# Kernel optimization log

Hardware: AMD Instinct MI355X
Metric: run time of the kernel (lower is better)

## Reference

```python
import jax, jax.numpy as jnp
import numpy as np

N = 262144      # total nodes in disjoint batch
E = 4194304     # total edges (COO)
G = 4096        # number of graphs
DIN = 1
CH = 32


def setup_inputs() -> dict:
    key = jax.random.key(0)
    ks = jax.random.split(key, 16)
    inp = {
        "x": jax.random.uniform(ks[0], (N, DIN), dtype=jnp.float32),
        "edge_src": jax.random.randint(ks[1], (E,), 0, N, dtype=jnp.int32),
        "edge_dst": jax.random.randint(ks[2], (E,), 0, N, dtype=jnp.int32),
        "edge_w": jax.random.uniform(ks[3], (E,), dtype=jnp.float32),  # normalized-adj values
        "seg": jnp.sort(jax.random.randint(ks[4], (N,), 0, G, dtype=jnp.int32)),
        "W1_1": jax.random.normal(ks[5], (DIN, CH), dtype=jnp.float32) * 0.5,
        "W2_1": jax.random.normal(ks[6], (DIN, CH), dtype=jnp.float32) * 0.5,
        "b1": jnp.zeros((CH,), jnp.float32),
        "W1_2": jax.random.normal(ks[7], (CH, CH), dtype=jnp.float32) * (1.0 / np.sqrt(CH)),
        "W2_2": jax.random.normal(ks[8], (CH, CH), dtype=jnp.float32) * (1.0 / np.sqrt(CH)),
        "b2": jnp.zeros((CH,), jnp.float32),
        "W1_3": jax.random.normal(ks[9], (CH, CH), dtype=jnp.float32) * (1.0 / np.sqrt(CH)),
        "W2_3": jax.random.normal(ks[10], (CH, CH), dtype=jnp.float32) * (1.0 / np.sqrt(CH)),
        "b3": jnp.zeros((CH,), jnp.float32),
        "Wd": jax.random.normal(ks[11], (CH, 1), dtype=jnp.float32) * (1.0 / np.sqrt(CH)),
        "bd": jnp.zeros((1,), jnp.float32),
    }
    return inp


def gcs_conv(x, src, dst, w, W1, W2, b):
    # GCSConv: out = relu(A_hat @ (x W1) + x W2 + b), A_hat sparse COO
    h = x @ W1                                   # [N, CH]
    msg = h[src] * w[:, None]                    # gather + edge weight [E, CH]
    agg = jax.ops.segment_sum(msg, dst, num_segments=N)  # scatter-add [N, CH]
    return jax.nn.relu(agg + x @ W2 + b)


def reference(x, edge_src, edge_dst, edge_w, seg,
              W1_1, W2_1, b1, W1_2, W2_2, b2, W1_3, W2_3, b3, Wd, bd):
    x = gcs_conv(x, edge_src, edge_dst, edge_w, W1_1, W2_1, b1)
    x = gcs_conv(x, edge_src, edge_dst, edge_w, W1_2, W2_2, b2)
    x = gcs_conv(x, edge_src, edge_dst, edge_w, W1_3, W2_3, b3)
    # GlobalAvgPool over graph segments
    sums = jax.ops.segment_sum(x, seg, num_segments=G)           # [G, CH]
    counts = jax.ops.segment_sum(jnp.ones((x.shape[0],), x.dtype), seg, num_segments=G)
    pooled = sums / jnp.maximum(counts, 1.0)[:, None]            # [G, CH]
    return jax.nn.sigmoid(pooled @ Wd + bd)                      # [G, 1]
```

## Files before the change

### kernel.cpp

```cpp
#include <hip/hip_runtime.h>
#include <hip/hip_bf16.h>
#include <hip/hip_fp8.h>

#define CH 32
#define BSHIFT 10
#define BNODES (1 << BSHIFT)
#define MAXBUK 256
#define P3_CHUNK 2048
#define CAPB_REC 17408
#define NT 32
#define CAP 768

__device__ __forceinline__ float fp8_to_f32(unsigned int b) {
    __hip_fp8_e4m3 v; v.__x = (__hip_fp8_storage_t)b; return (float)v;
}
__device__ __forceinline__ unsigned char f32_to_fp8(float f) {
    return (unsigned char)__hip_fp8_e4m3(f).__x;
}
__device__ __forceinline__ int2 nt_load_int2(const int2* p) {
    long long raw = __builtin_nontemporal_load(reinterpret_cast<const long long*>(p));
    return make_int2((int)(unsigned int)raw, (int)(raw >> 32));
}


__global__ void init_tails_kernel(int* __restrict__ bucketTail, int nbuk) {
    int tid = threadIdx.x;
    if (tid < nbuk) bucketTail[tid] = tid * CAPB_REC;
}

__global__ void bucket_scatter_kernel(const int* __restrict__ src, const int* __restrict__ dst,
                                      const float* __restrict__ w, int* __restrict__ bucketTail,
                                      int2* __restrict__ rec, int E, int nbuk) {
    __shared__ int cnt[MAXBUK], base[MAXBUK], offs[MAXBUK];
    int tid = threadIdx.x;
    int begin = blockIdx.x * P3_CHUNK;
    int end = min(begin + P3_CHUNK, E);
    if (tid < MAXBUK) cnt[tid] = 0;
    __syncthreads();
    for (int e = begin + tid; e < end; e += 256)
        atomicAdd(&cnt[dst[e] >> BSHIFT], 1);
    __syncthreads();
    if (tid < nbuk) {
        base[tid] = cnt[tid] ? atomicAdd(&bucketTail[tid], cnt[tid]) : 0;
        offs[tid] = 0;
    }
    __syncthreads();
    for (int e = begin + tid; e < end; e += 256) {
        int d = dst[e];
        int b = d >> BSHIFT;
        int p = base[b] + atomicAdd(&offs[b], 1);
        rec[p] = make_int2(src[e] | ((d & (BNODES - 1)) << 18), __float_as_int(w[e]));
    }
}

__global__ void bucket_scan2_kernel(const int* __restrict__ bucketTail, int* __restrict__ bucketStart,
                                    int* __restrict__ row_start, int nbuk, int N, int E) {
    __shared__ int l[MAXBUK];
    int tid = threadIdx.x;
    int v = (tid < nbuk) ? (bucketTail[tid] - tid * CAPB_REC) : 0;
    l[tid] = v;
    __syncthreads();
    for (int off = 1; off < MAXBUK; off <<= 1) {
        int t = (tid >= off) ? l[tid - off] : 0;
        __syncthreads();
        l[tid] += t;
        __syncthreads();
    }
    int ex = l[tid] - v;
    if (tid < nbuk) bucketStart[tid] = ex;
    if (tid == nbuk - 1) bucketStart[nbuk] = ex + v;
    if (tid == 0) row_start[N] = E;
}

__global__ void local_csr_kernel(const int2* __restrict__ rec, const int* __restrict__ bucketStart,
                                 const int* __restrict__ bucketTail,
                                 int* __restrict__ row_start, int2* __restrict__ colw, int N) {
    int b = blockIdx.x;
    int lo_rec = b * CAPB_REC, hi_rec = bucketTail[b];
    int dstBase = bucketStart[b];
    int nodeBase = b << BSHIFT;
    int nNodes = min(BNODES, N - nodeBase);
    __shared__ int deg[BNODES];
    __shared__ int rs[BNODES];
    __shared__ int l[256];
    int tid = threadIdx.x;
    for (int i = tid; i < BNODES; i += 256) deg[i] = 0;
    __syncthreads();
    for (int j = lo_rec + tid; j < hi_rec; j += 256)
        atomicAdd(&deg[rec[j].x >> 18], 1);
    __syncthreads();
    int i0 = tid * 4;
    int v0 = deg[i0], v1 = deg[i0 + 1], v2 = deg[i0 + 2], v3 = deg[i0 + 3];
    int tsum = v0 + v1 + v2 + v3;
    l[tid] = tsum;
    __syncthreads();
    for (int off = 1; off < 256; off <<= 1) {
        int t = (tid >= off) ? l[tid - off] : 0;
        __syncthreads();
        l[tid] += t;
        __syncthreads();
    }
    int ex = l[tid] - tsum;
    rs[i0] = ex; rs[i0 + 1] = ex + v0; rs[i0 + 2] = ex + v0 + v1; rs[i0 + 3] = ex + v0 + v1 + v2;
    __syncthreads();
    for (int i = tid; i < nNodes; i += 256) row_start[nodeBase + i] = dstBase + rs[i];
    for (int i = tid; i < BNODES; i += 256) deg[i] = 0;
    __syncthreads();
    for (int j = lo_rec + tid; j < hi_rec; j += 256) {
        int2 r = rec[j];
        int dl = r.x >> 18;
        int p = dstBase + rs[dl] + atomicAdd(&deg[dl], 1);
        colw[p] = make_int2(r.x & 0x3FFFF, r.y);
    }
}

__global__ void l1_fused_kernel(const float* __restrict__ x,
                                const int* __restrict__ row_start, const int2* __restrict__ colw,
                                const float* __restrict__ W11, const float* __restrict__ W21,
                                const float* __restrict__ b1, const float* __restrict__ W12,
                                float* __restrict__ x1, unsigned char* __restrict__ h2, int N) {
    __shared__ float w1s[CH][CH];
    __shared__ float xs[8][CH + 1];
    int tid = threadIdx.x;
    for (int t = tid; t < CH * CH; t += 256) w1s[t >> 5][t & 31] = W12[t];
    int ln = tid >> 5, c = tid & 31;
    int node = blockIdx.x * 8 + ln;
    float s = 0.f, xv = 0.f;
    if (node < N) {
        xv = x[node];
        int lo = row_start[node], hi = row_start[node + 1];
        for (int j = lo + c; j < hi; j += 32) {
            int2 cw = nt_load_int2(&colw[j]);
            s += __int_as_float(cw.y) * x[cw.x];
        }
    }
    for (int m = 1; m < 32; m <<= 1) s += __shfl_xor(s, m);
    float x1v = 0.f;
    if (node < N) {
        x1v = fmaxf(fmaf(s, W11[c], fmaf(xv, W21[c], b1[c])), 0.f);
        x1[(size_t)node * CH + c] = x1v;
    }
    xs[ln][c] = x1v;
    __syncthreads();
    if (node < N) {
        float a = 0.f;
#pragma unroll
        for (int k = 0; k < CH; k++) a = fmaf(xs[ln][k], w1s[k][c], a);
        h2[(size_t)node * CH + c] = f32_to_fp8(a);
    }
}

template <bool EMIT_H>
__global__ void gather_kernel(float* __restrict__ xio, const unsigned char* __restrict__ h,
                              const int* __restrict__ row_start, const int2* __restrict__ colw,
                              const float* __restrict__ W2, const float* __restrict__ b,
                              const float* __restrict__ W1next, unsigned char* __restrict__ hout,
                              int N) {
    __shared__ float w2s[CH][CH];
    __shared__ float w1s[EMIT_H ? CH : 1][CH];
    __shared__ float xs[NT][CH + 1];
    __shared__ int2 cws[CAP];
    int tid = threadIdx.x;
    int nodeBase = blockIdx.x * NT;

    for (int t = tid; t < CH * CH; t += 256) {
        w2s[t >> 5][t & 31] = W2[t];
        if (EMIT_H) w1s[t >> 5][t & 31] = W1next[t];
    }
    {
        int n = tid >> 5, c = tid & 31;
        for (int p = 0; p < NT / 8; p++) {
            int node = nodeBase + p * 8 + n;
            xs[p * 8 + n][c] = (node < N) ? __builtin_nontemporal_load(&xio[(size_t)node * CH + c]) : 0.f;
        }
    }
    int lo = row_start[min(nodeBase, N)];
    int hi = row_start[min(nodeBase + NT, N)];
    int total = hi - lo;
    int cnt = min(total, CAP);
    for (int t = tid; t < cnt; t += 256) cws[t] = nt_load_int2(&colw[lo + t]);
    __syncthreads();

    int grp = tid >> 4, l16 = tid & 15;
    int c0 = l16 * 2;
#pragma unroll
    for (int rep = 0; rep < NT / 16; rep++) {
        int nloc = rep * 16 + grp;
        int node = nodeBase + nloc;
        if (node < N) {
            int ls = row_start[node], le = row_start[node + 1];
            float a0 = b[c0], a1 = b[c0 + 1];
#pragma unroll
            for (int k = 0; k < CH; k++) {
                float xk = xs[nloc][k];
                float2 wk = *reinterpret_cast<const float2*>(&w2s[k][c0]);
                a0 = fmaf(xk, wk.x, a0);
                a1 = fmaf(xk, wk.y, a1);
            }
            if (total <= cnt) {
                int j = ls;
                for (; j + 4 <= le; j += 4) {
                    int2 e0 = cws[j - lo], e1 = cws[j + 1 - lo], e2 = cws[j + 2 - lo], e3 = cws[j + 3 - lo];
                    unsigned int p0 = *reinterpret_cast<const unsigned short*>(h + (size_t)e0.x * CH + c0);
                    unsigned int p1 = *reinterpret_cast<const unsigned short*>(h + (size_t)e1.x * CH + c0);
                    unsigned int p2 = *reinterpret_cast<const unsigned short*>(h + (size_t)e2.x * CH + c0);
                    unsigned int p3 = *reinterpret_cast<const unsigned short*>(h + (size_t)e3.x * CH + c0);
                    float w0 = __int_as_float(e0.y), w1 = __int_as_float(e1.y);
                    float w2 = __int_as_float(e2.y), w3 = __int_as_float(e3.y);
                    a0 = fmaf(w0, fp8_to_f32(p0 & 0xff), a0); a1 = fmaf(w0, fp8_to_f32(p0 >> 8), a1);
                    a0 = fmaf(w1, fp8_to_f32(p1 & 0xff), a0); a1 = fmaf(w1, fp8_to_f32(p1 >> 8), a1);
                    a0 = fmaf(w2, fp8_to_f32(p2 & 0xff), a0); a1 = fmaf(w2, fp8_to_f32(p2 >> 8), a1);
                    a0 = fmaf(w3, fp8_to_f32(p3 & 0xff), a0); a1 = fmaf(w3, fp8_to_f32(p3 >> 8), a1);
                }
                for (; j < le; j++) {
                    int2 e = cws[j - lo];
                    unsigned int p = *reinterpret_cast<const unsigned short*>(h + (size_t)e.x * CH + c0);
                    float wj = __int_as_float(e.y);
                    a0 = fmaf(wj, fp8_to_f32(p & 0xff), a0); a1 = fmaf(wj, fp8_to_f32(p >> 8), a1);
                }
            } else {
                for (int j = ls; j < le; j++) {
                    int2 e = nt_load_int2(&colw[j]);
                    unsigned int p = *reinterpret_cast<const unsigned short*>(h + (size_t)e.x * CH + c0);
                    float wj = __int_as_float(e.y);
                    a0 = fmaf(wj, fp8_to_f32(p & 0xff), a0); a1 = fmaf(wj, fp8_to_f32(p >> 8), a1);
                }
            }
            float r0 = fmaxf(a0, 0.f), r1 = fmaxf(a1, 0.f);
            size_t oidx = (size_t)node * CH + c0;
            __builtin_nontemporal_store(r0, &xio[oidx]);
            __builtin_nontemporal_store(r1, &xio[oidx + 1]);
            if (EMIT_H) { xs[nloc][c0] = r0; xs[nloc][c0 + 1] = r1; }
        }
    }
    if (EMIT_H) {
        __syncthreads();
#pragma unroll
        for (int rep = 0; rep < NT / 16; rep++) {
            int nloc = rep * 16 + grp;
            int node = nodeBase + nloc;
            if (node >= N) continue;
            float a0 = 0.f, a1 = 0.f;
#pragma unroll
            for (int k = 0; k < CH; k++) {
                float xk = xs[nloc][k];
                float2 wk = *reinterpret_cast<const float2*>(&w1s[k][c0]);
                a0 = fmaf(xk, wk.x, a0);
                a1 = fmaf(xk, wk.y, a1);
            }
            unsigned short pk = (unsigned short)f32_to_fp8(a0) |
                                ((unsigned short)f32_to_fp8(a1) << 8);
            __builtin_nontemporal_store(pk,
                reinterpret_cast<unsigned short*>(hout + (size_t)node * CH + c0));
        }
    }
}

__global__ void pool_head_kernel(const float* __restrict__ x3, const int* __restrict__ seg,
                                 const float* __restrict__ Wd, const float* __restrict__ bd,
                                 float* __restrict__ out, int N, int G) {
    int g = blockIdx.x;
    int tid = threadIdx.x;
    int lo = 0, hi = N;
    while (lo < hi) { int mid = (lo + hi) >> 1; if (seg[mid] < g) lo = mid + 1; else hi = mid; }
    int start = lo;
    hi = N;
    while (lo < hi) { int mid = (lo + hi) >> 1; if (seg[mid] < g + 1) lo = mid + 1; else hi = mid; }
    int end = lo;
    int half = tid >> 5, c = tid & 31;
    float s = 0.f;
    for (int nn = start + half; nn < end; nn += 2)
        s += __builtin_nontemporal_load(&x3[(size_t)nn * CH + c]);
    s += __shfl_xor(s, 32);
    float t = s * Wd[c];
    for (int m = 1; m < 32; m <<= 1) t += __shfl_xor(t, m);
    if (tid == 0) {
        float cntf = fmaxf((float)(end - start), 1.f);
        float logit = t / cntf + bd[0];
        out[g] = 1.f / (1.f + expf(-logit));
    }
}

extern "C" void kernel_launch(void* const* d_in, const int* in_sizes, int n_in,
                              void* d_out, int out_size, void* d_ws, size_t ws_size,
                              hipStream_t stream) {
    const float* x        = (const float*)d_in[0];
    const int*   edge_src = (const int*)d_in[1];
    const int*   edge_dst = (const int*)d_in[2];
    const float* edge_w   = (const float*)d_in[3];
    const int*   seg      = (const int*)d_in[4];
    const float* W1_1 = (const float*)d_in[5];
    const float* W2_1 = (const float*)d_in[6];
    const float* b1   = (const float*)d_in[7];
    const float* W1_2 = (const float*)d_in[8];
    const float* W2_2 = (const float*)d_in[9];
    const float* b2   = (const float*)d_in[10];
    const float* W1_3 = (const float*)d_in[11];
    const float* W2_3 = (const float*)d_in[12];
    const float* b3   = (const float*)d_in[13];
    const float* Wd   = (const float*)d_in[14];
    const float* bd   = (const float*)d_in[15];
    float* out = (float*)d_out;

    const int N = in_sizes[0];
    const int E = in_sizes[1];
    const int G = out_size;
    (void)ws_size; (void)n_in;

    const int nbuk = (N + BNODES - 1) >> BSHIFT;

    const size_t NB = (size_t)N * CH;
    float*           xbuf      = (float*)d_ws;
    int2*            rec       = (int2*)d_ws;
    unsigned char*   h8a       = (unsigned char*)(xbuf + NB);
    unsigned char*   h8b       = h8a + NB;
    int*             row_start = (int*)(h8b + NB);
    int2*            colw      = (int2*)(row_start + (N + 8));
    int*             bucketStart = (int*)(colw + E);
    int*             bucketTail  = bucketStart + MAXBUK + 4;

    const int BLK = 256;

    init_tails_kernel<<<1, BLK, 0, stream>>>(bucketTail, nbuk);
    bucket_scatter_kernel<<<(E + P3_CHUNK - 1) / P3_CHUNK, BLK, 0, stream>>>(
        edge_src, edge_dst, edge_w, bucketTail, rec, E, nbuk);
    bucket_scan2_kernel<<<1, BLK, 0, stream>>>(bucketTail, bucketStart, row_start, nbuk, N, E);
    local_csr_kernel<<<nbuk, BLK, 0, stream>>>(rec, bucketStart, bucketTail, row_start, colw, N);

    l1_fused_kernel<<<(N + 7) / 8, BLK, 0, stream>>>(x, row_start, colw,
                                                     W1_1, W2_1, b1, W1_2, xbuf, h8a, N);
    gather_kernel<true><<<(N + NT - 1) / NT, BLK, 0, stream>>>(xbuf, h8a, row_start, colw,
                                                               W2_2, b2, W1_3, h8b, N);
    gather_kernel<false><<<(N + NT - 1) / NT, BLK, 0, stream>>>(xbuf, h8b, row_start, colw,
                                                                W2_3, b3, nullptr, nullptr, N);

    pool_head_kernel<<<G, 64, 0, stream>>>(xbuf, seg, Wd, bd, out, N, G);
}
```

Before: 473.9 us.

## Split gather into two source-half passes to improve cache locality of fp8 features

```diff
diff --git a/kernel.cpp b/kernel.cpp
--- a/kernel.cpp
+++ b/kernel.cpp
@@ -6,7 +6,7 @@
 #define BSHIFT 10
 #define BNODES (1 << BSHIFT)
 #define MAXBUK 256
-#define P3_CHUNK 2048
+#define P3_CHUNK 8192
 #define CAPB_REC 17408
 #define NT 32
 #define CAP 768
@@ -74,24 +74,28 @@
 
 __global__ void local_csr_kernel(const int2* __restrict__ rec, const int* __restrict__ bucketStart,
                                  const int* __restrict__ bucketTail,
-                                 int* __restrict__ row_start, int2* __restrict__ colw, int N) {
+                                 int* __restrict__ row_start, int* __restrict__ row_mid,
+                                 int2* __restrict__ colw, int N, int halfN) {
     int b = blockIdx.x;
     int lo_rec = b * CAPB_REC, hi_rec = bucketTail[b];
     int dstBase = bucketStart[b];
     int nodeBase = b << BSHIFT;
     int nNodes = min(BNODES, N - nodeBase);
-    __shared__ int deg[BNODES];
-    __shared__ int rs[BNODES];
+    __shared__ int degA[BNODES], degB[BNODES], rs[BNODES], bofs[BNODES];
     __shared__ int l[256];
     int tid = threadIdx.x;
-    for (int i = tid; i < BNODES; i += 256) deg[i] = 0;
-    __syncthreads();
-    for (int j = lo_rec + tid; j < hi_rec; j += 256)
-        atomicAdd(&deg[rec[j].x >> 18], 1);
+    for (int i = tid; i < BNODES; i += 256) { degA[i] = 0; degB[i] = 0; }
+    __syncthreads();
+    for (int j = lo_rec + tid; j < hi_rec; j += 256) {
+        int rx = rec[j].x;
+        int dl = rx >> 18;
+        atomicAdd(((rx & 0x3FFFF) < halfN) ? &degA[dl] : &degB[dl], 1);
+    }
     __syncthreads();
     int i0 = tid * 4;
-    int v0 = deg[i0], v1 = deg[i0 + 1], v2 = deg[i0 + 2], v3 = deg[i0 + 3];
-    int tsum = v0 + v1 + v2 + v3;
+    int t0 = degA[i0] + degB[i0], t1 = degA[i0 + 1] + degB[i0 + 1];
+    int t2 = degA[i0 + 2] + degB[i0 + 2], t3 = degA[i0 + 3] + degB[i0 + 3];
+    int tsum = t0 + t1 + t2 + t3;
     l[tid] = tsum;
     __syncthreads();
     for (int off = 1; off < 256; off <<= 1) {
@@ -101,16 +105,23 @@
         __syncthreads();
     }
     int ex = l[tid] - tsum;
-    rs[i0] = ex; rs[i0 + 1] = ex + v0; rs[i0 + 2] = ex + v0 + v1; rs[i0 + 3] = ex + v0 + v1 + v2;
-    __syncthreads();
-    for (int i = tid; i < nNodes; i += 256) row_start[nodeBase + i] = dstBase + rs[i];
-    for (int i = tid; i < BNODES; i += 256) deg[i] = 0;
+    rs[i0] = ex; rs[i0 + 1] = ex + t0; rs[i0 + 2] = ex + t0 + t1; rs[i0 + 3] = ex + t0 + t1 + t2;
+    __syncthreads();
+    for (int i = tid; i < BNODES; i += 256) bofs[i] = rs[i] + degA[i];
+    __syncthreads();
+    for (int i = tid; i < nNodes; i += 256) {
+        row_start[nodeBase + i] = dstBase + rs[i];
+        row_mid[nodeBase + i]   = dstBase + bofs[i];
+    }
+    for (int i = tid; i < BNODES; i += 256) { degA[i] = 0; degB[i] = 0; }
     __syncthreads();
     for (int j = lo_rec + tid; j < hi_rec; j += 256) {
         int2 r = rec[j];
         int dl = r.x >> 18;
-        int p = dstBase + rs[dl] + atomicAdd(&deg[dl], 1);
-        colw[p] = make_int2(r.x & 0x3FFFF, r.y);
+        int s = r.x & 0x3FFFF;
+        int p = (s < halfN) ? dstBase + rs[dl] + atomicAdd(&degA[dl], 1)
+                            : dstBase + bofs[dl] + atomicAdd(&degB[dl], 1);
+        colw[p] = make_int2(s, r.y);
     }
 }
 
@@ -150,24 +161,25 @@
     }
 }
 
-template <bool EMIT_H>
+template <int PHASE, bool EMIT_H>
 __global__ void gather_kernel(float* __restrict__ xio, const unsigned char* __restrict__ h,
-                              const int* __restrict__ row_start, const int2* __restrict__ colw,
+                              const int* __restrict__ row_start, const int* __restrict__ row_mid,
+                              const int2* __restrict__ colw,
                               const float* __restrict__ W2, const float* __restrict__ b,
                               const float* __restrict__ W1next, unsigned char* __restrict__ hout,
                               int N) {
-    __shared__ float w2s[CH][CH];
+    __shared__ float w2s[PHASE == 0 ? CH : 1][CH];
     __shared__ float w1s[EMIT_H ? CH : 1][CH];
     __shared__ float xs[NT][CH + 1];
     __shared__ int2 cws[CAP];
     int tid = threadIdx.x;
     int nodeBase = blockIdx.x * NT;
 
-    for (int t = tid; t < CH * CH; t += 256) {
-        w2s[t >> 5][t & 31] = W2[t];
-        if (EMIT_H) w1s[t >> 5][t & 31] = W1next[t];
-    }
-    {
+    if (PHASE == 0)
+        for (int t = tid; t < CH * CH; t += 256) w2s[t >> 5][t & 31] = W2[t];
+    if (EMIT_H)
+        for (int t = tid; t < CH * CH; t += 256) w1s[t >> 5][t & 31] = W1next[t];
+    if (PHASE == 0) {
         int n = tid >> 5, c = tid & 31;
         for (int p = 0; p < NT / 8; p++) {
             int node = nodeBase + p * 8 + n;
@@ -188,14 +200,23 @@
         int nloc = rep * 16 + grp;
         int node = nodeBase + nloc;
         if (node < N) {
-            int ls = row_start[node], le = row_start[node + 1];
-            float a0 = b[c0], a1 = b[c0 + 1];
-#pragma unroll
-            for (int k = 0; k < CH; k++) {
-                float xk = xs[nloc][k];
-                float2 wk = *reinterpret_cast<const float2*>(&w2s[k][c0]);
-                a0 = fmaf(xk, wk.x, a0);
-                a1 = fmaf(xk, wk.y, a1);
+            int ls, le;
+            if (PHASE == 0) { ls = row_start[node]; le = row_mid[node]; }
+            else            { ls = row_mid[node];   le = row_start[node + 1]; }
+            float a0, a1;
+            if (PHASE == 0) {
+                a0 = b[c0]; a1 = b[c0 + 1];
+#pragma unroll
+                for (int k = 0; k < CH; k++) {
+                    float xk = xs[nloc][k];
+                    float2 wk = *reinterpret_cast<const float2*>(&w2s[k][c0]);
+                    a0 = fmaf(xk, wk.x, a0);
+                    a1 = fmaf(xk, wk.y, a1);
+                }
+            } else {
+                size_t oidx = (size_t)node * CH + c0;
+                a0 = __builtin_nontemporal_load(&xio[oidx]);
+                a1 = __builtin_nontemporal_load(&xio[oidx + 1]);
             }
             if (total <= cnt) {
                 int j = ls;
@@ -226,11 +247,16 @@
                     a0 = fmaf(wj, fp8_to_f32(p & 0xff), a0); a1 = fmaf(wj, fp8_to_f32(p >> 8), a1);
                 }
             }
-            float r0 = fmaxf(a0, 0.f), r1 = fmaxf(a1, 0.f);
             size_t oidx = (size_t)node * CH + c0;
-            __builtin_nontemporal_store(r0, &xio[oidx]);
-            __builtin_nontemporal_store(r1, &xio[oidx + 1]);
-            if (EMIT_H) { xs[nloc][c0] = r0; xs[nloc][c0 + 1] = r1; }
+            if (PHASE == 0) {
+                __builtin_nontemporal_store(a0, &xio[oidx]);
+                __builtin_nontemporal_store(a1, &xio[oidx + 1]);
+            } else {
+                float r0 = fmaxf(a0, 0.f), r1 = fmaxf(a1, 0.f);
+                __builtin_nontemporal_store(r0, &xio[oidx]);
+                __builtin_nontemporal_store(r1, &xio[oidx + 1]);
+                if (EMIT_H) { xs[nloc][c0] = r0; xs[nloc][c0 + 1] = r1; }
+            }
         }
     }
     if (EMIT_H) {
@@ -308,6 +334,7 @@
     (void)ws_size; (void)n_in;
 
     const int nbuk = (N + BNODES - 1) >> BSHIFT;
+    const int halfN = N >> 1;
 
     const size_t NB = (size_t)N * CH;
     float*           xbuf      = (float*)d_ws;
@@ -315,24 +342,31 @@
     unsigned char*   h8a       = (unsigned char*)(xbuf + NB);
     unsigned char*   h8b       = h8a + NB;
     int*             row_start = (int*)(h8b + NB);
-    int2*            colw      = (int2*)(row_start + (N + 8));
+    int*             row_mid   = row_start + (N + 8);
+    int2*            colw      = (int2*)(row_mid + (N + 8));
     int*             bucketStart = (int*)(colw + E);
     int*             bucketTail  = bucketStart + MAXBUK + 4;
 
     const int BLK = 256;
+    const int NGB = (N + NT - 1) / NT;
 
     init_tails_kernel<<<1, BLK, 0, stream>>>(bucketTail, nbuk);
     bucket_scatter_kernel<<<(E + P3_CHUNK - 1) / P3_CHUNK, BLK, 0, stream>>>(
         edge_src, edge_dst, edge_w, bucketTail, rec, E, nbuk);
     bucket_scan2_kernel<<<1, BLK, 0, stream>>>(bucketTail, bucketStart, row_start, nbuk, N, E);
-    local_csr_kernel<<<nbuk, BLK, 0, stream>>>(rec, bucketStart, bucketTail, row_start, colw, N);
+    local_csr_kernel<<<nbuk, BLK, 0, stream>>>(rec, bucketStart, bucketTail,
+                                               row_start, row_mid, colw, N, halfN);
 
     l1_fused_kernel<<<(N + 7) / 8, BLK, 0, stream>>>(x, row_start, colw,
                                                      W1_1, W2_1, b1, W1_2, xbuf, h8a, N);
-    gather_kernel<true><<<(N + NT - 1) / NT, BLK, 0, stream>>>(xbuf, h8a, row_start, colw,
-                                                               W2_2, b2, W1_3, h8b, N);
-    gather_kernel<false><<<(N + NT - 1) / NT, BLK, 0, stream>>>(xbuf, h8b, row_start, colw,
-                                                                W2_3, b3, nullptr, nullptr, N);
+    gather_kernel<0, false><<<NGB, BLK, 0, stream>>>(xbuf, h8a, row_start, row_mid, colw,
+                                                     W2_2, b2, nullptr, nullptr, N);
+    gather_kernel<1, true><<<NGB, BLK, 0, stream>>>(xbuf, h8a, row_start, row_mid, colw,
+                                                    W2_2, b2, W1_3, h8b, N);
+    gather_kernel<0, false><<<NGB, BLK, 0, stream>>>(xbuf, h8b, row_start, row_mid, colw,
+                                                     W2_3, b3, nullptr, nullptr, N);
+    gather_kernel<1, false><<<NGB, BLK, 0, stream>>>(xbuf, h8b, row_start, row_mid, colw,
+                                                     W2_3, b3, nullptr, nullptr, N);
 
     pool_head_kernel<<<G, 64, 0, stream>>>(xbuf, seg, Wd, bd, out, N, G);
 }
```

Measured after the change: 469.5 us. About the same (-0.9%).
